# Kernel tuning notes

Hardware: AMD Instinct MI355X
Metric: run time of the kernel (lower is better)

The kernel has to match this reference:

```python
import jax, jax.numpy as jnp
import numpy as np

B, C_IN, V, C_OUT, K = 4, 64, 50000, 128, 7


def setup_inputs() -> dict:
    key = jax.random.key(0)
    k1, k2, k3, k4 = jax.random.split(key, 4)
    x = jax.random.normal(k1, (B, C_IN, V, 1), dtype=jnp.float32)
    # Gi: per-vertex [self, n1, n2, n3] indices (random neighbors, in-range)
    Gi = jax.random.randint(k2, (B, V, 4), 0, V, dtype=jnp.int64)
    # Conv2d(in, out, kernel=(1,7)) weight collapsed to [out, in, 7]
    W = jax.random.normal(k3, (C_OUT, C_IN, K), dtype=jnp.float32) * 0.05
    b = jax.random.normal(k4, (C_OUT,), dtype=jnp.float32) * 0.05
    return {"x": x, "Gi": Gi, "W": W, "b": b}


def reference(x, Gi, W, b):
    xs = x[..., 0]  # [B, C, V]  (squeeze(-1))
    Bx, C, Vx = xs.shape
    # prepend zero-padding column (index 0 after Gi+1 maps padded -1 entries)
    xp = jnp.concatenate([jnp.zeros((Bx, C, 1), xs.dtype), xs], axis=2)  # [B,C,V+1]
    gi = Gi + 1
    # gather per batch: f[b,c,v,j] = xp[b,c,gi[b,v,j]]
    f = jax.vmap(lambda xb, gb: xb[:, gb])(xp, gi)  # [B, C, V, 4]
    f0, f1, f2, f3 = f[..., 0], f[..., 1], f[..., 2], f[..., 3]
    G = jnp.stack([
        f0,
        f1 + f2 + f3,                                        # symm_oper 1
        f1 * f2 * f3,                                        # symm_oper 2
        f1 * f2 + f1 * f3 + f2 * f3,                         # symm_oper 3
        f1 * f1 + f2 * f2 + f3 * f3,                         # symm_oper 4
        jnp.abs(f1 - f2) + jnp.abs(f1 - f3) + jnp.abs(f2 - f3),  # symm_oper 5
        f1 * f1 * f1 + f2 * f2 * f2 + f3 * f3 * f3,          # symm_oper 6
    ], axis=3)  # [B, C, V, 7]
    # conv2d with kernel (1,7), no padding -> width collapses to 1
    out = jnp.einsum('bcvk,ock->bov', G, W) + b[None, :, None]
    return out[..., None]  # [B, C_out, V, 1]
```

## Files before the change

kernel.cpp:

```cpp
#include <hip/hip_runtime.h>
#include <cstdint>
#include <cstddef>

#define BB   4
#define CIN  64
#define VV   50000
#define COUT 128
#define NV   32
#define KTOT 448
#define KT   14
#define PITCH 456

typedef __attribute__((ext_vector_type(8))) short    short8;
typedef __attribute__((ext_vector_type(8))) _Float16 half8;
typedef __attribute__((ext_vector_type(4))) float    f32x4;

__device__ _Float16       g_xt[(size_t)BB * VV * CIN];
__device__ unsigned short g_wb[KT * 8 * 64 * 8];

__device__ inline unsigned short f2h(float f) {
    union { _Float16 h; unsigned short u; } cv;
    cv.h = (_Float16)f;
    return cv.u;
}

__global__ __launch_bounds__(256) void transpose_k(const float* __restrict__ x,
                                                   const float* __restrict__ W) {
    if (blockIdx.y == 0 && blockIdx.x < (KT * 8 * 64 + 255) / 256) {
        int idx = blockIdx.x * 256 + threadIdx.x;
        if (idx < KT * 8 * 64) {
            int lane = idx & 63;
            int mt   = (idx >> 6) & 7;
            int kt   = idx >> 9;
            int m    = mt * 16 + (lane & 15);
            int kb   = kt * 32 + (lane >> 4) * 8;
            union { unsigned short s[8]; short8 v; } u;
#pragma unroll
            for (int j = 0; j < 8; j++) {
                int kk = kb + j;
                int c  = kk & 63;
                int k  = kk >> 6;
                u.s[j] = f2h(W[((size_t)m * CIN + c) * 7 + k]);
            }
            *(short8*)&g_wb[(size_t)idx * 8] = u.v;
        }
    }

    __shared__ float tile[64][65];
    int b  = blockIdx.y;
    int v0 = blockIdx.x * 64;
    int t  = threadIdx.x;
    int tv = t & 15;
    int tc = t >> 4;
#pragma unroll
    for (int i = 0; i < 4; i++) {
        int c = tc + 16 * i;
        int v = v0 + tv * 4;
        const float* src = x + ((size_t)b * CIN + c) * VV + v;
        f32x4 f;
        if (v + 3 < VV) {
            f = __builtin_nontemporal_load((const f32x4*)src);
        } else {
            f[0] = v + 0 < VV ? src[0] : 0.f;
            f[1] = v + 1 < VV ? src[1] : 0.f;
            f[2] = v + 2 < VV ? src[2] : 0.f;
            f[3] = v + 3 < VV ? src[3] : 0.f;
        }
        tile[c][tv * 4 + 0] = f[0];
        tile[c][tv * 4 + 1] = f[1];
        tile[c][tv * 4 + 2] = f[2];
        tile[c][tv * 4 + 3] = f[3];
    }
    __syncthreads();
    int c8  = t & 7;
    int tvv = t >> 3;
#pragma unroll
    for (int i = 0; i < 2; i++) {
        int v = v0 + tvv + 32 * i;
        if (v < VV) {
            union { _Float16 h[8]; short8 s; } u;
#pragma unroll
            for (int j = 0; j < 8; j++)
                u.h[j] = (_Float16)tile[c8 * 8 + j][tvv + 32 * i];
            *(short8*)(g_xt + ((size_t)b * VV + v) * CIN + c8 * 8) = u.s;
        }
    }
}

__device__ inline void feats(float f0, float f1, float f2, float f3, float* g) {
    g[0] = f0;
    g[1] = f1 + f2 + f3;
    float p12 = f1 * f2, p13 = f1 * f3, p23 = f2 * f3;
    g[2] = p12 * f3;
    g[3] = p12 + p13 + p23;
    g[4] = f1 * f1 + f2 * f2 + f3 * f3;
    g[5] = fabsf(f1 - f2) + fabsf(f1 - f3) + fabsf(f2 - f3);
    g[6] = f1 * f1 * f1 + f2 * f2 * f2 + f3 * f3 * f3;
}

__global__ __launch_bounds__(256) void mesh_k(
        const void* __restrict__ Gi, const float* __restrict__ bias,
        float* __restrict__ out) {
    __shared__ _Float16 Gl[NV * PITCH];
    __shared__ int Sidx[NV][4];

    int b  = blockIdx.y;
    int v0 = blockIdx.x * NV;
    int t  = threadIdx.x;

    const unsigned* gu = (const unsigned*)Gi;
    bool is64 = ((gu[1] | gu[3] | gu[5] | gu[7]) == 0u);

    if (t < NV * 4) {
        int vv = t >> 2, j = t & 3;
        int v  = v0 + vv;
        long long val = 0;
        if (v < VV) {
            size_t gb = ((size_t)b * VV + v) * 4 + j;
            val = is64 ? __builtin_nontemporal_load((const long long*)Gi + gb)
                       : (long long)__builtin_nontemporal_load((const int*)Gi + gb);
        }
        Sidx[vv][j] = (int)(val < 0 ? 0 : (val >= VV ? VV - 1 : val));
    }
    __syncthreads();

    int c8   = t & 7;
    int slot = t >> 3;
    int J[4];
#pragma unroll
    for (int j = 0; j < 4; ++j) J[j] = Sidx[slot][j];

    const _Float16* base = g_xt + (size_t)b * VV * CIN + c8 * 8;
    half8 F[4];
#pragma unroll
    for (int j = 0; j < 4; ++j)
        F[j] = *(const half8*)(base + (size_t)J[j] * CIN);

    union { _Float16 h[8]; short8 s; } u[7];
#pragma unroll
    for (int i = 0; i < 8; ++i) {
        float g7[7];
        feats((float)F[0][i], (float)F[1][i], (float)F[2][i], (float)F[3][i], g7);
#pragma unroll
        for (int k = 0; k < 7; ++k) u[k].h[i] = (_Float16)g7[k];
    }
    _Float16* grow = &Gl[slot * PITCH + c8 * 8];
#pragma unroll
    for (int k = 0; k < 7; ++k)
        *(short8*)(grow + k * 64) = u[k].s;
    __syncthreads();

    int w    = t >> 6;
    int lane = t & 63;
    int l15  = lane & 15;
    int q    = lane >> 4;

    f32x4 acc[2][2] = {};

    const half8* wb = (const half8*)g_wb;
#pragma unroll 2
    for (int kt = 0; kt < KT; ++kt) {
        half8 a0 = wb[(kt * 8 + 2 * w    ) * 64 + lane];
        half8 a1 = wb[(kt * 8 + 2 * w + 1) * 64 + lane];
        half8 b0 = *(const half8*)&Gl[(l15     ) * PITCH + kt * 32 + q * 8];
        half8 b1 = *(const half8*)&Gl[(l15 + 16) * PITCH + kt * 32 + q * 8];
        acc[0][0] = __builtin_amdgcn_mfma_f32_16x16x32_f16(a0, b0, acc[0][0], 0, 0, 0);
        acc[0][1] = __builtin_amdgcn_mfma_f32_16x16x32_f16(a0, b1, acc[0][1], 0, 0, 0);
        acc[1][0] = __builtin_amdgcn_mfma_f32_16x16x32_f16(a1, b0, acc[1][0], 0, 0, 0);
        acc[1][1] = __builtin_amdgcn_mfma_f32_16x16x32_f16(a1, b1, acc[1][1], 0, 0, 0);
    }

#pragma unroll
    for (int mt = 0; mt < 2; ++mt) {
        int o = 32 * w + mt * 16 + q * 4;
        float bs[4];
#pragma unroll
        for (int r = 0; r < 4; ++r) bs[r] = bias[o + r];
#pragma unroll
        for (int n = 0; n < 2; ++n) {
            int v = v0 + n * 16 + l15;
            if (v < VV) {
                float* po = out + ((size_t)b * COUT + o) * VV + v;
#pragma unroll
                for (int r = 0; r < 4; ++r)
                    __builtin_nontemporal_store(acc[mt][n][r] + bs[r], po + (size_t)r * VV);
            }
        }
    }
}

extern "C" void kernel_launch(void* const* d_in, const int* in_sizes, int n_in,
                              void* d_out, int out_size, void* d_ws, size_t ws_size,
                              hipStream_t stream) {
    const float* x    = (const float*)d_in[0];
    const void*  Gi   = d_in[1];
    const float* W    = (const float*)d_in[2];
    const float* bias = (const float*)d_in[3];
    float* out        = (float*)d_out;

    dim3 gt((VV + 63) / 64, BB);
    transpose_k<<<gt, 256, 0, stream>>>(x, W);
    dim3 gm((VV + NV - 1) / NV, BB);
    mesh_k<<<gm, 256, 0, stream>>>(Gi, bias, out);
}
```

Before: 197.5 us.

## Process three vertex tiles per block with prefetched neighbor gathers

Each mesh block now handles three 32-vertex tiles instead of one. All index rows are loaded up front with vector loads and no shared-memory staging. The gathers for the next tile are issued before computing the current tile's features and MFMA, to hide gather latency. This also amortises block launch and the weight/index setup, and sets a launch-bounds occupancy hint. The cost is more registers and fewer blocks, which can reduce parallelism and tail balance.

Result: no change. 201.0 us (+1.8%).

```diff
diff --git a/kernel.cpp b/kernel.cpp
--- a/kernel.cpp
+++ b/kernel.cpp
@@ -7,13 +7,17 @@
 #define VV   50000
 #define COUT 128
 #define NV   32
+#define TPB  3
+#define NTILES 1563
 #define KTOT 448
 #define KT   14
 #define PITCH 456
 
-typedef __attribute__((ext_vector_type(8))) short    short8;
-typedef __attribute__((ext_vector_type(8))) _Float16 half8;
-typedef __attribute__((ext_vector_type(4))) float    f32x4;
+typedef __attribute__((ext_vector_type(8))) short     short8;
+typedef __attribute__((ext_vector_type(8))) _Float16  half8;
+typedef __attribute__((ext_vector_type(4))) float     f32x4;
+typedef __attribute__((ext_vector_type(2))) long long llx2;
+typedef __attribute__((ext_vector_type(4))) int       i32x4;
 
 __device__ _Float16       g_xt[(size_t)BB * VV * CIN];
 __device__ unsigned short g_wb[KT * 8 * 64 * 8];
@@ -98,95 +102,127 @@
     g[6] = f1 * f1 * f1 + f2 * f2 * f2 + f3 * f3 * f3;
 }
 
-__global__ __launch_bounds__(256) void mesh_k(
+__global__ __launch_bounds__(256, 5) void mesh_k(
         const void* __restrict__ Gi, const float* __restrict__ bias,
         float* __restrict__ out) {
     __shared__ _Float16 Gl[NV * PITCH];
-    __shared__ int Sidx[NV][4];
-
-    int b  = blockIdx.y;
-    int v0 = blockIdx.x * NV;
-    int t  = threadIdx.x;
+
+    int b     = blockIdx.y;
+    int t     = threadIdx.x;
+    int c8    = t & 7;
+    int slot  = t >> 3;
+    int tile0 = blockIdx.x * TPB;
 
     const unsigned* gu = (const unsigned*)Gi;
     bool is64 = ((gu[1] | gu[3] | gu[5] | gu[7]) == 0u);
 
-    if (t < NV * 4) {
-        int vv = t >> 2, j = t & 3;
-        int v  = v0 + vv;
-        long long val = 0;
-        if (v < VV) {
-            size_t gb = ((size_t)b * VV + v) * 4 + j;
-            val = is64 ? __builtin_nontemporal_load((const long long*)Gi + gb)
-                       : (long long)__builtin_nontemporal_load((const int*)Gi + gb);
-        }
-        Sidx[vv][j] = (int)(val < 0 ? 0 : (val >= VV ? VV - 1 : val));
-    }
-    __syncthreads();
-
-    int c8   = t & 7;
-    int slot = t >> 3;
-    int J[4];
-#pragma unroll
-    for (int j = 0; j < 4; ++j) J[j] = Sidx[slot][j];
-
-    const _Float16* base = g_xt + (size_t)b * VV * CIN + c8 * 8;
-    half8 F[4];
-#pragma unroll
-    for (int j = 0; j < 4; ++j)
-        F[j] = *(const half8*)(base + (size_t)J[j] * CIN);
-
-    union { _Float16 h[8]; short8 s; } u[7];
-#pragma unroll
-    for (int i = 0; i < 8; ++i) {
-        float g7[7];
-        feats((float)F[0][i], (float)F[1][i], (float)F[2][i], (float)F[3][i], g7);
-#pragma unroll
-        for (int k = 0; k < 7; ++k) u[k].h[i] = (_Float16)g7[k];
-    }
-    _Float16* grow = &Gl[slot * PITCH + c8 * 8];
-#pragma unroll
-    for (int k = 0; k < 7; ++k)
-        *(short8*)(grow + k * 64) = u[k].s;
-    __syncthreads();
+    int idx[TPB][4];
+    if (is64) {
+        llx2 ra[TPB], rb[TPB];
+#pragma unroll
+        for (int i = 0; i < TPB; i++) {
+            int v = (tile0 + i) * NV + slot;
+            if (v < VV) {
+                const llx2* p = (const llx2*)Gi + ((size_t)b * VV + v) * 2;
+                ra[i] = __builtin_nontemporal_load(p);
+                rb[i] = __builtin_nontemporal_load(p + 1);
+            } else {
+                ra[i] = (llx2){0, 0};
+                rb[i] = (llx2){0, 0};
+            }
+        }
+#pragma unroll
+        for (int i = 0; i < TPB; i++) {
+            long long v4[4] = { ra[i][0], ra[i][1], rb[i][0], rb[i][1] };
+#pragma unroll
+            for (int j = 0; j < 4; j++)
+                idx[i][j] = (int)(v4[j] < 0 ? 0 : (v4[j] >= VV ? VV - 1 : v4[j]));
+        }
+    } else {
+        i32x4 r[TPB];
+#pragma unroll
+        for (int i = 0; i < TPB; i++) {
+            int v = (tile0 + i) * NV + slot;
+            r[i] = (v < VV) ? __builtin_nontemporal_load((const i32x4*)Gi + ((size_t)b * VV + v))
+                            : (i32x4){0, 0, 0, 0};
+        }
+#pragma unroll
+        for (int i = 0; i < TPB; i++) {
+#pragma unroll
+            for (int j = 0; j < 4; j++) {
+                int vj = r[i][j];
+                idx[i][j] = vj < 0 ? 0 : (vj >= VV ? VV - 1 : vj);
+            }
+        }
+    }
+
+    const _Float16* xb = g_xt + (size_t)b * VV * CIN + c8 * 8;
 
     int w    = t >> 6;
     int lane = t & 63;
     int l15  = lane & 15;
     int q    = lane >> 4;
 
-    f32x4 acc[2][2] = {};
-
-    const half8* wb = (const half8*)g_wb;
+    half8 Fa[4], Fb[4];
+#pragma unroll
+    for (int j = 0; j < 4; ++j)
+        Fa[j] = *(const half8*)(xb + (size_t)idx[0][j] * CIN);
+
+    auto tile_body = [&](int i, half8 (&Fc)[4], half8 (&Fn)[4]) {
+        if (i + 1 < TPB) {
+#pragma unroll
+            for (int j = 0; j < 4; ++j)
+                Fn[j] = *(const half8*)(xb + (size_t)idx[i + 1][j] * CIN);
+        }
+        union { _Float16 h[8]; short8 s; } u[7];
+#pragma unroll
+        for (int ii = 0; ii < 8; ++ii) {
+            float g7[7];
+            feats((float)Fc[0][ii], (float)Fc[1][ii], (float)Fc[2][ii],
+                  (float)Fc[3][ii], g7);
+#pragma unroll
+            for (int k = 0; k < 7; ++k) u[k].h[ii] = (_Float16)g7[k];
+        }
+        if (i > 0) __syncthreads();
+        _Float16* grow = &Gl[slot * PITCH + c8 * 8];
+#pragma unroll
+        for (int k = 0; k < 7; ++k)
+            *(short8*)(grow + k * 64) = u[k].s;
+        __syncthreads();
+
+        f32x4 acc[2][2] = {};
+        const half8* wb = (const half8*)g_wb;
 #pragma unroll 2
-    for (int kt = 0; kt < KT; ++kt) {
-        half8 a0 = wb[(kt * 8 + 2 * w    ) * 64 + lane];
-        half8 a1 = wb[(kt * 8 + 2 * w + 1) * 64 + lane];
-        half8 b0 = *(const half8*)&Gl[(l15     ) * PITCH + kt * 32 + q * 8];
-        half8 b1 = *(const half8*)&Gl[(l15 + 16) * PITCH + kt * 32 + q * 8];
-        acc[0][0] = __builtin_amdgcn_mfma_f32_16x16x32_f16(a0, b0, acc[0][0], 0, 0, 0);
-        acc[0][1] = __builtin_amdgcn_mfma_f32_16x16x32_f16(a0, b1, acc[0][1], 0, 0, 0);
-        acc[1][0] = __builtin_amdgcn_mfma_f32_16x16x32_f16(a1, b0, acc[1][0], 0, 0, 0);
-        acc[1][1] = __builtin_amdgcn_mfma_f32_16x16x32_f16(a1, b1, acc[1][1], 0, 0, 0);
-    }
-
-#pragma unroll
-    for (int mt = 0; mt < 2; ++mt) {
-        int o = 32 * w + mt * 16 + q * 4;
-        float bs[4];
-#pragma unroll
-        for (int r = 0; r < 4; ++r) bs[r] = bias[o + r];
-#pragma unroll
-        for (int n = 0; n < 2; ++n) {
-            int v = v0 + n * 16 + l15;
-            if (v < VV) {
-                float* po = out + ((size_t)b * COUT + o) * VV + v;
-#pragma unroll
-                for (int r = 0; r < 4; ++r)
-                    __builtin_nontemporal_store(acc[mt][n][r] + bs[r], po + (size_t)r * VV);
-            }
-        }
-    }
+        for (int kt = 0; kt < KT; ++kt) {
+            half8 a0 = wb[(kt * 8 + 2 * w    ) * 64 + lane];
+            half8 a1 = wb[(kt * 8 + 2 * w + 1) * 64 + lane];
+            half8 b0 = *(const half8*)&Gl[(l15     ) * PITCH + kt * 32 + q * 8];
+            half8 b1 = *(const half8*)&Gl[(l15 + 16) * PITCH + kt * 32 + q * 8];
+            acc[0][0] = __builtin_amdgcn_mfma_f32_16x16x32_f16(a0, b0, acc[0][0], 0, 0, 0);
+            acc[0][1] = __builtin_amdgcn_mfma_f32_16x16x32_f16(a0, b1, acc[0][1], 0, 0, 0);
+            acc[1][0] = __builtin_amdgcn_mfma_f32_16x16x32_f16(a1, b0, acc[1][0], 0, 0, 0);
+            acc[1][1] = __builtin_amdgcn_mfma_f32_16x16x32_f16(a1, b1, acc[1][1], 0, 0, 0);
+        }
+
+        int vt = (tile0 + i) * NV;
+#pragma unroll
+        for (int mt = 0; mt < 2; ++mt) {
+            int o = 32 * w + mt * 16 + q * 4;
+#pragma unroll
+            for (int r = 0; r < 4; ++r) {
+                float bsr = bias[o + r];
+                float* po = out + ((size_t)b * COUT + o + r) * VV + vt + l15;
+                if (vt + l15 < VV)
+                    __builtin_nontemporal_store(acc[mt][0][r] + bsr, po);
+                if (vt + 16 + l15 < VV)
+                    __builtin_nontemporal_store(acc[mt][1][r] + bsr, po + 16);
+            }
+        }
+    };
+
+    tile_body(0, Fa, Fb);
+    tile_body(1, Fb, Fa);
+    tile_body(2, Fa, Fb);
 }
 
 extern "C" void kernel_launch(void* const* d_in, const int* in_sizes, int n_in,
@@ -200,6 +236,6 @@
 
     dim3 gt((VV + 63) / 64, BB);
     transpose_k<<<gt, 256, 0, stream>>>(x, W);
-    dim3 gm((VV + NV - 1) / NV, BB);
+    dim3 gm((NTILES + TPB - 1) / TPB, BB);
     mesh_k<<<gm, 256, 0, stream>>>(Gi, bias, out);
 }
```
